# Kernel tuning notes

Measured on AMD Instinct MI355X. Metric: run time of the kernel, lower is better.

## Reference

```python
import jax, jax.numpy as jnp
import numpy as np

NEG = -10000.0
PAD_ID = 0


def setup_inputs() -> dict:
    key = jax.random.key(0)
    ks = jax.random.split(key, 9)
    B, S, D, K, L = 32, 256, 512, 8, 64
    word_rep = jax.random.normal(ks[0], (B, S, D), jnp.float32)
    mask = jnp.ones((B, S), jnp.int32)
    # conv_w[k,:,:,:k+1] are the taps of Conv1d(D, D, k+1); padded to width K for a single tensor
    conv_w = jax.random.normal(ks[1], (K, D, D, K), jnp.float32) * 0.02
    conv_b = jax.random.normal(ks[2], (K, D), jnp.float32) * 0.02
    cls_w = jax.random.normal(ks[3], (L, D), jnp.float32) * 0.02
    cls_b = jax.random.normal(ks[4], (L,), jnp.float32) * 0.02
    T = jax.random.normal(ks[5], (L, L), jnp.float32) * 0.01
    T = T.at[PAD_ID, :].set(NEG).at[:, PAD_ID].set(NEG)
    T_from_BEGIN = jax.random.normal(ks[6], (L,), jnp.float32) * 0.01
    T_from_BEGIN = T_from_BEGIN.at[PAD_ID].set(NEG)
    T_to_END = jax.random.normal(ks[7], (L,), jnp.float32) * 0.01
    T_to_END = T_to_END.at[PAD_ID].set(NEG)
    return dict(word_rep=word_rep, mask=mask, conv_w=conv_w, conv_b=conv_b,
                cls_w=cls_w, cls_b=cls_b, T=T, T_from_BEGIN=T_from_BEGIN, T_to_END=T_to_END)


def _semicrf(word_rep, mask, conv_w, conv_b, cls_w, cls_b, T, T_from_BEGIN, T_to_END):
    B, S, D = word_rep.shape
    K = conv_w.shape[0]
    L = cls_w.shape[0]
    # ---- segment representations: Conv1d(D, D, k+1) placed at [:, k:, k, :] ----
    x = jnp.transpose(word_rep, (0, 2, 1))  # [B, D, S]
    word_seq_rep = jnp.zeros((B, S, K, D), word_rep.dtype)
    for k in range(K):
        w = conv_w[k, :, :, :k + 1]  # [D_out, D_in, k+1]
        out = jax.lax.conv_general_dilated(
            x, w, window_strides=(1,), padding='VALID',
            dimension_numbers=('NCH', 'OIH', 'NCH')) + conv_b[k][None, :, None]  # [B, D, S-k]
        word_seq_rep = word_seq_rep.at[:, k:, k, :].set(jnp.transpose(out, (0, 2, 1)))
    # ---- label scores ----
    label_score = jnp.einsum('bskd,ld->bskl', word_seq_rep, cls_w) + cls_b  # [B,S,K,L]
    label_score = label_score.at[..., PAD_ID].set(NEG)
    seg_ok = jnp.arange(K)[None, :] <= jnp.arange(S)[:, None]  # [S, K]: segment of len k+1 valid only if t >= k
    mask3 = (mask[:, :, None] == 1) & seg_ok[None]              # [B, S, K]
    label_score = jnp.where(mask3[..., None], label_score, NEG)
    # ---- semi-CRF forward recursion over t (sequential scan) ----
    # buf[:, j] holds log_alpha at position t-1-j for j in [0, K)
    def step(buf, inp):
        ls_t, m_t, t = inp  # [B,K,L], [B,K], scalar
        lse_prev = jax.nn.logsumexp(buf, axis=2)                                  # over kk -> [B,K,L']
        tmp = jax.nn.logsumexp(T[None, None, :, :] + lse_prev[:, :, None, :], axis=3)  # over l' -> [B,K,L]
        rec = jnp.where(m_t[..., None], ls_t + tmp, NEG)
        begin = ls_t + T_from_BEGIN[None, None, :]
        karr = jnp.arange(K)[None, :, None]
        row = jnp.where(karr == t, begin, jnp.where(karr > t, NEG, rec))  # [B,K,L]
        buf = jnp.concatenate([row[:, None], buf[:, :-1]], axis=1)
        return buf, row

    buf0 = jnp.full((B, K, K, L), NEG, word_rep.dtype)
    xs = (jnp.transpose(label_score, (1, 0, 2, 3)), jnp.transpose(mask3, (1, 0, 2)), jnp.arange(S))
    _, rows = jax.lax.scan(step, buf0, xs)
    log_alpha = jnp.concatenate(
        [jnp.transpose(rows, (1, 0, 2, 3)), jnp.full((B, 1, K, L), NEG, word_rep.dtype)], axis=1)  # [B,S+1,K,L]
    # ---- log partition: gather log_alpha at last token per segment length, add T_to_END, logsumexp ----
    lengths = jnp.sum(mask, axis=1)                                   # [B]
    idxs = lengths[:, None] - (jnp.arange(K)[None, :] + 1)            # [B,K]
    idxs = jnp.where(idxs >= 0, idxs, S - 1)
    idx_arr = jnp.broadcast_to(idxs[:, None, :, None], (B, 1, K, L))
    g = jnp.take_along_axis(log_alpha, idx_arr, axis=1)[:, 0]         # [B,K,L]
    scores = g + T_to_END[None, None, :]
    return jax.nn.logsumexp(scores.reshape(B, K * L), axis=1)         # [B]


def reference(word_rep, mask, conv_w, conv_b, cls_w, cls_b, T, T_from_BEGIN, T_to_END):
    return _semicrf(word_rep, mask, conv_w, conv_b, cls_w, cls_b, T, T_from_BEGIN, T_to_END)
```

## Files before the change

### kernel.cpp

```cpp
#include <hip/hip_runtime.h>
#include <hip/hip_bf16.h>

#define NEGV (-10000.0f)
constexpr int B_ = 32, S_ = 256, D_ = 512, K_ = 8, L_ = 64;

typedef __bf16 bf16_t;
typedef bf16_t bf16x8 __attribute__((ext_vector_type(8)));
typedef float f32x4 __attribute__((ext_vector_type(4)));

__device__ __forceinline__ float u2f(unsigned int u) {
  union { unsigned int u; float f; } x; x.u = u; return x.f;
}
__device__ __forceinline__ unsigned int f2bfbits(float f) {
  union { bf16_t h; unsigned short u; } x; x.h = (bf16_t)f; return (unsigned int)x.u;
}

__global__ __launch_bounds__(256) void cast_kernel(const float* __restrict__ wr,
                                                   bf16_t* __restrict__ Awr,
                                                   const float* __restrict__ cls_w,
                                                   bf16_t* __restrict__ clsb) {
  const int bid = blockIdx.x;
  if (bid < 2048) {
    const int i = (bid * 256 + threadIdx.x) * 8;
    const float4 a = *(const float4*)(wr + i);
    const float4 b = *(const float4*)(wr + i + 4);
    bf16x8 o;
    o[0] = (bf16_t)a.x; o[1] = (bf16_t)a.y; o[2] = (bf16_t)a.z; o[3] = (bf16_t)a.w;
    o[4] = (bf16_t)b.x; o[5] = (bf16_t)b.y; o[6] = (bf16_t)b.z; o[7] = (bf16_t)b.w;
    *(bf16x8*)(Awr + i) = o;
  } else {
    const int i = ((bid - 2048) * 256 + threadIdx.x) * 8;
    const float4 a = *(const float4*)(cls_w + i);
    const float4 b = *(const float4*)(cls_w + i + 4);
    bf16x8 o;
    o[0] = (bf16_t)a.x; o[1] = (bf16_t)a.y; o[2] = (bf16_t)a.z; o[3] = (bf16_t)a.w;
    o[4] = (bf16_t)b.x; o[5] = (bf16_t)b.y; o[6] = (bf16_t)b.z; o[7] = (bf16_t)b.w;
    *(bf16x8*)(clsb + i) = o;
  }
}

__global__ __launch_bounds__(256) void w2_kernel(const float* __restrict__ conv_w,
                                                 const bf16_t* __restrict__ clsb,
                                                 bf16_t* __restrict__ Vt) {
  const int k = blockIdx.y;
  const int m0 = blockIdx.x * 128;
  const int tid = threadIdx.x;
  const int w = tid >> 6, lane = tid & 63;
  const int wm = w & 1, wn = w >> 1;
  const int lrow = lane & 15, quad = lane >> 4;
  const float* A = conv_w + (size_t)k * 2097152;
  f32x4 acc[4][2] = {};
#pragma unroll 2
  for (int kk = 0; kk < 16; kk++) {
    const int d0 = kk * 32 + quad * 8;
    const bf16x8 b0 = *(const bf16x8*)(clsb + (wn * 32 + lrow) * 512 + kk * 32 + quad * 8);
    const bf16x8 b1 = *(const bf16x8*)(clsb + (wn * 32 + 16 + lrow) * 512 + kk * 32 + quad * 8);
#pragma unroll
    for (int mi = 0; mi < 4; mi++) {
      const int ih = m0 + wm * 64 + mi * 16 + lrow;
      const float* ap = A + (size_t)d0 * 4096 + ih;
      bf16x8 a;
      a[0] = (bf16_t)ap[0 * 4096]; a[1] = (bf16_t)ap[1 * 4096];
      a[2] = (bf16_t)ap[2 * 4096]; a[3] = (bf16_t)ap[3 * 4096];
      a[4] = (bf16_t)ap[4 * 4096]; a[5] = (bf16_t)ap[5 * 4096];
      a[6] = (bf16_t)ap[6 * 4096]; a[7] = (bf16_t)ap[7 * 4096];
      acc[mi][0] = __builtin_amdgcn_mfma_f32_16x16x32_bf16(a, b0, acc[mi][0], 0, 0, 0);
      acc[mi][1] = __builtin_amdgcn_mfma_f32_16x16x32_bf16(a, b1, acc[mi][1], 0, 0, 0);
    }
  }
#pragma unroll
  for (int mi = 0; mi < 4; mi++) {
#pragma unroll
    for (int dd = 0; dd < 4; dd++) {
      const int ih = m0 + wm * 64 + mi * 16 + quad * 4 + dd;
      const int i = ih >> 3, h = ih & 7;
      const int o = k - h;
      if (o >= 0) {
#pragma unroll
        for (int ni = 0; ni < 2; ni++) {
          const int l = wn * 32 + ni * 16 + lrow;
          Vt[(size_t)(k * 64 + l) * 4096 + o * 512 + i] = (bf16_t)acc[mi][ni][dd];
        }
      }
    }
  }
}

__global__ __launch_bounds__(256) void bias2_kernel(const float* __restrict__ conv_b,
                                                    const float* __restrict__ cls_w,
                                                    const float* __restrict__ cls_b,
                                                    float* __restrict__ bias2) {
  const int k = blockIdx.x;
  const int tid = threadIdx.x;
  const int l = tid & 63, c = tid >> 6;
  __shared__ float partb[4][64];
  float s = 0.f;
  for (int d = c * 128; d < c * 128 + 128; d++)
    s += conv_b[k * D_ + d] * cls_w[l * D_ + d];
  partb[c][l] = s;
  __syncthreads();
  if (tid < 64)
    bias2[k * 64 + tid] = cls_b[tid] + partb[0][tid] + partb[1][tid] + partb[2][tid] + partb[3][tid];
}

__global__ __launch_bounds__(256) void ls_mfma(const bf16_t* __restrict__ Awr,
                                               const bf16_t* __restrict__ Vt,
                                               const float* __restrict__ bias2,
                                               const int* __restrict__ mask,
                                               unsigned int* __restrict__ ELSd) {
  constexpr int LDA = 520;
  __shared__ __align__(16) bf16_t As[71 * LDA];
  const int tid = threadIdx.x;
  const int m0 = blockIdx.x * 64;
  const int y = blockIdx.y;
  const int w = tid >> 6, lane = tid & 63;
  const int lrow = lane & 15, quad = lane >> 4;
  const int tblA[4] = {7, 0, 5, 2}, tblB[4] = {6, 1, 4, 3};
  const int kS = (y == 0) ? tblA[w] : tblB[w];

  for (int c = tid; c < 71 * 64; c += 256) {
    const int row = c >> 6, col8 = c & 63;
    int src = m0 - 7 + row;
    if (src < 0) src = 0;
    const uint4 v = *(const uint4*)(Awr + (size_t)src * 512 + col8 * 8);
    *(uint4*)(&As[row * LDA + col8 * 8]) = v;
  }
  __syncthreads();

  f32x4 acc[4][4] = {};
  const int NJ = 16 * (kS + 1);
  const bf16_t* vbase = Vt + (size_t)(kS * 64 + lrow) * 4096 + quad * 8;
#pragma unroll 2
  for (int j = 0; j < NJ; j++) {
    const int o = j >> 4;
    const int col = (j & 15) * 32;
    bf16x8 bfr[4];
#pragma unroll
    for (int ni = 0; ni < 4; ni++)
      bfr[ni] = *(const bf16x8*)(vbase + (size_t)(ni * 16) * 4096 + j * 32);
    const int abase = (lrow + 7 - o) * LDA + col + quad * 8;
#pragma unroll
    for (int mi = 0; mi < 4; mi++) {
      const bf16x8 a = *(const bf16x8*)(&As[abase + mi * 16 * LDA]);
#pragma unroll
      for (int ni = 0; ni < 4; ni++)
        acc[mi][ni] = __builtin_amdgcn_mfma_f32_16x16x32_bf16(a, bfr[ni], acc[mi][ni], 0, 0, 0);
    }
  }

  __syncthreads();
  unsigned short* buf = (unsigned short*)As;
#pragma unroll
  for (int ni = 0; ni < 4; ni++) {
    const int l = ni * 16 + lrow;
    const float bn = bias2[kS * 64 + l];
#pragma unroll
    for (int mi = 0; mi < 4; mi++) {
#pragma unroll
      for (int d = 0; d < 4; d++) {
        const int ml = mi * 16 + quad * 4 + d;
        const int m = m0 + ml;
        const int t = m & 255;
        const bool mok = (mask[m] == 1) && (t >= kS) && (l != 0);
        const float e = mok ? __expf(acc[mi][ni][d] + bn) : 0.f;
        buf[w * 4096 + ml * 64 + l] = (unsigned short)f2bfbits(e);
      }
    }
  }
  __syncthreads();
#pragma unroll
  for (int g = 0; g < 2; g++) {
    const int plane = g * 2 + y;
    const unsigned short* lo = buf + (g * 2) * 4096;
    const unsigned short* hi = buf + (g * 2 + 1) * 4096;
#pragma unroll
    for (int it = 0; it < 16; it++) {
      const int idx = it * 256 + tid;
      const unsigned int dw = (unsigned int)lo[idx] | ((unsigned int)hi[idx] << 16);
      ELSd[((size_t)plane * 8192 + m0 + (idx >> 6)) * 64 + (idx & 63)] = dw;
    }
  }
}

__global__ __launch_bounds__(256, 1) void dp_kernel(const float* __restrict__ T,
                                                    const float* __restrict__ Tfb_g,
                                                    const unsigned int* __restrict__ ELSd,
                                                    float* __restrict__ Mg_lin,
                                                    float* __restrict__ cs_g) {
  const int b = blockIdx.x, tid = threadIdx.x;
  const int w = tid >> 6, l = tid & 63;
  __shared__ __align__(16) float ebuf[64];
  __shared__ float part[4][72];
  __shared__ __align__(16) float pmax[4];
  f32x4 rTq[4];
#pragma unroll
  for (int q = 0; q < 4; q++) {
#pragma unroll
    for (int e = 0; e < 4; e++) rTq[q][e] = __expf(T[l * 64 + w * 16 + q * 4 + e]);
  }
  float mh0 = 0.f, mh1 = 0.f, mh2 = 0.f, mh3 = 0.f, mh4 = 0.f, mh5 = 0.f, mh6 = 0.f, mh7 = 0.f;
  float c = 0.f;
  const unsigned int* e0p = ELSd + ((size_t)0 * 8192 + b * 256) * 64 + l;
  const unsigned int* e1p = ELSd + ((size_t)1 * 8192 + b * 256) * 64 + l;
  const unsigned int* e2p = ELSd + ((size_t)2 * 8192 + b * 256) * 64 + l;
  const unsigned int* e3p = ELSd + ((size_t)3 * 8192 + b * 256) * 64 + l;
  uint4 r0, r1, r2, r3;
  if (w == 0) {
    mh0 = __expf(Tfb_g[l]);
    r0 = make_uint4(e0p[0 * 64], e1p[0 * 64], e2p[0 * 64], e3p[0 * 64]);
    r1 = make_uint4(e0p[1 * 64], e1p[1 * 64], e2p[1 * 64], e3p[1 * 64]);
    r2 = make_uint4(e0p[2 * 64], e1p[2 * 64], e2p[2 * 64], e3p[2 * 64]);
    r3 = make_uint4(e0p[3 * 64], e1p[3 * 64], e2p[3 * 64], e3p[3 * 64]);
  }
  for (int t4 = 0; t4 < 256; t4 += 4) {
#pragma unroll
    for (int u = 0; u < 4; u++) {
      const int t = t4 + u;
      if (w == 0) {
        if (t > 0) {
          const float p0 = part[0][l], p1 = part[1][l], p2 = part[2][l], p3 = part[3][l];
          const float m4 = (p0 + p1) + (p2 + p3);
          if ((t & 3) == 0) {
            const f32x4 pm = *(const f32x4*)pmax;
            float S = fmaxf(fmaxf(pm[0], pm[1]), fmaxf(pm[2], pm[3]));
            S = fmaxf(S, 1e-30f);
            const float inv = __builtin_amdgcn_rcpf(S);
            c += __logf(S);
            mh7 = mh6 * inv; mh6 = mh5 * inv; mh5 = mh4 * inv; mh4 = mh3 * inv;
            mh3 = mh2 * inv; mh2 = mh1 * inv; mh1 = mh0 * inv; mh0 = m4 * inv;
          } else {
            mh7 = mh6; mh6 = mh5; mh5 = mh4; mh4 = mh3;
            mh3 = mh2; mh2 = mh1; mh1 = mh0; mh0 = m4;
          }
        }
        const uint4 q = (u == 0) ? r0 : (u == 1) ? r1 : (u == 2) ? r2 : r3;
        const float f7 = u2f(q.x << 16), fk0 = u2f(q.x & 0xFFFF0000u);
        const float f6 = u2f(q.y << 16), fk1 = u2f(q.y & 0xFFFF0000u);
        const float f5 = u2f(q.z << 16), fk2 = u2f(q.z & 0xFFFF0000u);
        const float f4 = u2f(q.w << 16), fk3 = u2f(q.w & 0xFFFF0000u);
        const float e = ((fk0 * mh0 + fk1 * mh1) + (fk2 * mh2 + fk3 * mh3)) +
                        ((f4 * mh4 + f5 * mh5) + (f6 * mh6 + f7 * mh7));
        ebuf[l] = e;
        int nt = t + 4; if (nt > 255) nt = 255;
        const uint4 nv = make_uint4(e0p[(size_t)nt * 64], e1p[(size_t)nt * 64],
                                    e2p[(size_t)nt * 64], e3p[(size_t)nt * 64]);
        if (u == 0) r0 = nv; else if (u == 1) r1 = nv; else if (u == 2) r2 = nv; else r3 = nv;
      } else if (w == 1) {
        if (t > 0) {
          const float p0 = part[0][l], p1 = part[1][l], p2 = part[2][l], p3 = part[3][l];
          const float m4 = (p0 + p1) + (p2 + p3);
          Mg_lin[((size_t)b * 256 + (t - 1)) * 64 + l] = m4;
          if (l == 0) cs_g[b * 256 + (t - 1)] = c;
          if ((t & 3) == 0) {
            const f32x4 pm = *(const f32x4*)pmax;
            float S = fmaxf(fmaxf(pm[0], pm[1]), fmaxf(pm[2], pm[3]));
            S = fmaxf(S, 1e-30f);
            c += __logf(S);
          }
        }
      }
      __syncthreads();
      {
        const f32x4* evp = (const f32x4*)ebuf;
        const f32x4 v0 = evp[w * 4 + 0], v1 = evp[w * 4 + 1];
        const f32x4 v2 = evp[w * 4 + 2], v3 = evp[w * 4 + 3];
        f32x4 s01 = rTq[0] * v0 + rTq[1] * v1;
        f32x4 s23 = rTq[2] * v2 + rTq[3] * v3;
        const f32x4 sv = s01 + s23;
        part[w][l] = (sv[0] + sv[1]) + (sv[2] + sv[3]);
        const f32x4 mx = __builtin_elementwise_max(__builtin_elementwise_max(v0, v1),
                                                   __builtin_elementwise_max(v2, v3));
        if (l == 0) pmax[w] = fmaxf(fmaxf(mx[0], mx[1]), fmaxf(mx[2], mx[3]));
      }
      __syncthreads();
    }
  }
  if (w == 1) {
    const float p0 = part[0][l], p1 = part[1][l], p2 = part[2][l], p3 = part[3][l];
    const float m4 = (p0 + p1) + (p2 + p3);
    Mg_lin[((size_t)b * 256 + 255) * 64 + l] = m4;
    if (l == 0) cs_g[b * 256 + 255] = c;
  }
}

__global__ __launch_bounds__(64) void final_kernel(const int* __restrict__ mask,
                                                   const float* __restrict__ Tfb_g,
                                                   const float* __restrict__ T2e_g,
                                                   const unsigned int* __restrict__ ELSd,
                                                   const float* __restrict__ Mg_lin,
                                                   const float* __restrict__ cs_g,
                                                   float* __restrict__ out) {
  const int b = blockIdx.x, lane = threadIdx.x;
  int lenp = 0;
  for (int s = lane; s < S_; s += 64) lenp += (mask[b * S_ + s] == 1) ? 1 : 0;
#pragma unroll
  for (int off = 32; off > 0; off >>= 1) lenp += __shfl_xor(lenp, off);
  const int len = lenp;
  const float t2e = T2e_g[lane];
  float vals[8];
  float mx = -3.4e38f;
#pragma unroll
  for (int k = 0; k < 8; k++) {
    int tk = len - 1 - k;
    if (tk < 0) tk = S_ - 1;
    float g;
    if (k > tk) {
      g = NEGV;
    } else {
      const int p = (k < 4) ? k : (7 - k);
      const unsigned int dw = ELSd[((size_t)p * 8192 + b * 256 + tk) * 64 + lane];
      const float elsv = (k < 4) ? u2f(dw & 0xFFFF0000u) : u2f(dw << 16);
      const float ls = (elsv > 0.f) ? __logf(elsv) : NEGV;
      if (k == tk) {
        g = ls + Tfb_g[lane];
      } else if (mask[b * S_ + tk] == 1) {
        const int u = tk - 1 - k;
        const float mlin = Mg_lin[((size_t)b * S_ + u) * 64 + lane];
        const float M = (mlin > 0.f) ? (__logf(mlin) + cs_g[b * S_ + u]) : -1e30f;
        g = ls + M;
      } else {
        g = NEGV;
      }
    }
    const float v = g + t2e;
    vals[k] = v;
    mx = fmaxf(mx, v);
  }
#pragma unroll
  for (int off = 32; off > 0; off >>= 1) mx = fmaxf(mx, __shfl_xor(mx, off));
  float s = 0.f;
#pragma unroll
  for (int k = 0; k < 8; k++) s += __expf(vals[k] - mx);
#pragma unroll
  for (int off = 32; off > 0; off >>= 1) s += __shfl_xor(s, off);
  if (lane == 0) out[b] = __logf(s) + mx;
}

extern "C" void kernel_launch(void* const* d_in, const int* in_sizes, int n_in,
                              void* d_out, int out_size, void* d_ws, size_t ws_size,
                              hipStream_t stream) {
  const float* wr     = (const float*)d_in[0];
  const int*   mask   = (const int*)d_in[1];
  const float* conv_w = (const float*)d_in[2];
  const float* conv_b = (const float*)d_in[3];
  const float* cls_w  = (const float*)d_in[4];
  const float* cls_b  = (const float*)d_in[5];
  const float* T      = (const float*)d_in[6];
  const float* Tfb    = (const float*)d_in[7];
  const float* T2e    = (const float*)d_in[8];
  float* out = (float*)d_out;

  float* ws = (float*)d_ws;
  bf16_t* Vt    = (bf16_t*)ws;
  bf16_t* Awr   = (bf16_t*)(ws + 1048576);
  float*  bias2 = ws + 3145728;
  unsigned int* ELSd = (unsigned int*)(ws + 3146240);
  float*  Mg    = ws + 5243392;
  float*  cs    = ws + 5767680;
  bf16_t* clsb  = (bf16_t*)(ws + 5775872);

  cast_kernel<<<2064, 256, 0, stream>>>(wr, Awr, cls_w, clsb);
  w2_kernel<<<dim3(32, 8), 256, 0, stream>>>(conv_w, clsb, Vt);
  bias2_kernel<<<8, 256, 0, stream>>>(conv_b, cls_w, cls_b, bias2);
  ls_mfma<<<dim3(128, 2), 256, 0, stream>>>(Awr, Vt, bias2, mask, ELSd);
  dp_kernel<<<32, 256, 0, stream>>>(T, Tfb, ELSd, Mg, cs);
  final_kernel<<<32, 64, 0, stream>>>(mask, Tfb, T2e, ELSd, Mg, cs, out);
}
```

Baseline: 304.4 us.

## Fold fp32-to-bf16 casts into consumers and halve ls_mfma row tile

```diff
diff --git a/kernel.cpp b/kernel.cpp
--- a/kernel.cpp
+++ b/kernel.cpp
@@ -14,33 +14,15 @@
 __device__ __forceinline__ unsigned int f2bfbits(float f) {
   union { bf16_t h; unsigned short u; } x; x.h = (bf16_t)f; return (unsigned int)x.u;
 }
-
-__global__ __launch_bounds__(256) void cast_kernel(const float* __restrict__ wr,
-                                                   bf16_t* __restrict__ Awr,
-                                                   const float* __restrict__ cls_w,
-                                                   bf16_t* __restrict__ clsb) {
-  const int bid = blockIdx.x;
-  if (bid < 2048) {
-    const int i = (bid * 256 + threadIdx.x) * 8;
-    const float4 a = *(const float4*)(wr + i);
-    const float4 b = *(const float4*)(wr + i + 4);
-    bf16x8 o;
-    o[0] = (bf16_t)a.x; o[1] = (bf16_t)a.y; o[2] = (bf16_t)a.z; o[3] = (bf16_t)a.w;
-    o[4] = (bf16_t)b.x; o[5] = (bf16_t)b.y; o[6] = (bf16_t)b.z; o[7] = (bf16_t)b.w;
-    *(bf16x8*)(Awr + i) = o;
-  } else {
-    const int i = ((bid - 2048) * 256 + threadIdx.x) * 8;
-    const float4 a = *(const float4*)(cls_w + i);
-    const float4 b = *(const float4*)(cls_w + i + 4);
-    bf16x8 o;
-    o[0] = (bf16_t)a.x; o[1] = (bf16_t)a.y; o[2] = (bf16_t)a.z; o[3] = (bf16_t)a.w;
-    o[4] = (bf16_t)b.x; o[5] = (bf16_t)b.y; o[6] = (bf16_t)b.z; o[7] = (bf16_t)b.w;
-    *(bf16x8*)(clsb + i) = o;
-  }
+__device__ __forceinline__ bf16x8 cvt8(const float4 a, const float4 b) {
+  bf16x8 o;
+  o[0] = (bf16_t)a.x; o[1] = (bf16_t)a.y; o[2] = (bf16_t)a.z; o[3] = (bf16_t)a.w;
+  o[4] = (bf16_t)b.x; o[5] = (bf16_t)b.y; o[6] = (bf16_t)b.z; o[7] = (bf16_t)b.w;
+  return o;
 }
 
 __global__ __launch_bounds__(256) void w2_kernel(const float* __restrict__ conv_w,
-                                                 const bf16_t* __restrict__ clsb,
+                                                 const float* __restrict__ cls_w,
                                                  bf16_t* __restrict__ Vt) {
   const int k = blockIdx.y;
   const int m0 = blockIdx.x * 128;
@@ -53,8 +35,10 @@
 #pragma unroll 2
   for (int kk = 0; kk < 16; kk++) {
     const int d0 = kk * 32 + quad * 8;
-    const bf16x8 b0 = *(const bf16x8*)(clsb + (wn * 32 + lrow) * 512 + kk * 32 + quad * 8);
-    const bf16x8 b1 = *(const bf16x8*)(clsb + (wn * 32 + 16 + lrow) * 512 + kk * 32 + quad * 8);
+    const float* c0p = cls_w + (wn * 32 + lrow) * 512 + kk * 32 + quad * 8;
+    const float* c1p = cls_w + (wn * 32 + 16 + lrow) * 512 + kk * 32 + quad * 8;
+    const bf16x8 b0 = cvt8(*(const float4*)c0p, *(const float4*)(c0p + 4));
+    const bf16x8 b1 = cvt8(*(const float4*)c1p, *(const float4*)(c1p + 4));
 #pragma unroll
     for (int mi = 0; mi < 4; mi++) {
       const int ih = m0 + wm * 64 + mi * 16 + lrow;
@@ -103,31 +87,32 @@
     bias2[k * 64 + tid] = cls_b[tid] + partb[0][tid] + partb[1][tid] + partb[2][tid] + partb[3][tid];
 }
 
-__global__ __launch_bounds__(256) void ls_mfma(const bf16_t* __restrict__ Awr,
+__global__ __launch_bounds__(256) void ls_mfma(const float* __restrict__ wr,
                                                const bf16_t* __restrict__ Vt,
                                                const float* __restrict__ bias2,
                                                const int* __restrict__ mask,
                                                unsigned int* __restrict__ ELSd) {
   constexpr int LDA = 520;
-  __shared__ __align__(16) bf16_t As[71 * LDA];
+  __shared__ __align__(16) bf16_t As[39 * LDA];
   const int tid = threadIdx.x;
-  const int m0 = blockIdx.x * 64;
+  const int m0 = blockIdx.x * 32;
   const int y = blockIdx.y;
   const int w = tid >> 6, lane = tid & 63;
   const int lrow = lane & 15, quad = lane >> 4;
   const int tblA[4] = {7, 0, 5, 2}, tblB[4] = {6, 1, 4, 3};
   const int kS = (y == 0) ? tblA[w] : tblB[w];
 
-  for (int c = tid; c < 71 * 64; c += 256) {
+  for (int c = tid; c < 39 * 64; c += 256) {
     const int row = c >> 6, col8 = c & 63;
     int src = m0 - 7 + row;
     if (src < 0) src = 0;
-    const uint4 v = *(const uint4*)(Awr + (size_t)src * 512 + col8 * 8);
-    *(uint4*)(&As[row * LDA + col8 * 8]) = v;
+    const float* p = wr + (size_t)src * 512 + col8 * 8;
+    const bf16x8 o = cvt8(*(const float4*)p, *(const float4*)(p + 4));
+    *(bf16x8*)(&As[row * LDA + col8 * 8]) = o;
   }
   __syncthreads();
 
-  f32x4 acc[4][4] = {};
+  f32x4 acc[2][4] = {};
   const int NJ = 16 * (kS + 1);
   const bf16_t* vbase = Vt + (size_t)(kS * 64 + lrow) * 4096 + quad * 8;
 #pragma unroll 2
@@ -140,7 +125,7 @@
       bfr[ni] = *(const bf16x8*)(vbase + (size_t)(ni * 16) * 4096 + j * 32);
     const int abase = (lrow + 7 - o) * LDA + col + quad * 8;
 #pragma unroll
-    for (int mi = 0; mi < 4; mi++) {
+    for (int mi = 0; mi < 2; mi++) {
       const bf16x8 a = *(const bf16x8*)(&As[abase + mi * 16 * LDA]);
 #pragma unroll
       for (int ni = 0; ni < 4; ni++)
@@ -155,7 +140,7 @@
     const int l = ni * 16 + lrow;
     const float bn = bias2[kS * 64 + l];
 #pragma unroll
-    for (int mi = 0; mi < 4; mi++) {
+    for (int mi = 0; mi < 2; mi++) {
 #pragma unroll
       for (int d = 0; d < 4; d++) {
         const int ml = mi * 16 + quad * 4 + d;
@@ -163,7 +148,7 @@
         const int t = m & 255;
         const bool mok = (mask[m] == 1) && (t >= kS) && (l != 0);
         const float e = mok ? __expf(acc[mi][ni][d] + bn) : 0.f;
-        buf[w * 4096 + ml * 64 + l] = (unsigned short)f2bfbits(e);
+        buf[w * 2048 + ml * 64 + l] = (unsigned short)f2bfbits(e);
       }
     }
   }
@@ -171,10 +156,10 @@
 #pragma unroll
   for (int g = 0; g < 2; g++) {
     const int plane = g * 2 + y;
-    const unsigned short* lo = buf + (g * 2) * 4096;
-    const unsigned short* hi = buf + (g * 2 + 1) * 4096;
-#pragma unroll
-    for (int it = 0; it < 16; it++) {
+    const unsigned short* lo = buf + (g * 2) * 2048;
+    const unsigned short* hi = buf + (g * 2 + 1) * 2048;
+#pragma unroll
+    for (int it = 0; it < 8; it++) {
       const int idx = it * 256 + tid;
       const unsigned int dw = (unsigned int)lo[idx] | ((unsigned int)hi[idx] << 16);
       ELSd[((size_t)plane * 8192 + m0 + (idx >> 6)) * 64 + (idx & 63)] = dw;
@@ -352,17 +337,14 @@
 
   float* ws = (float*)d_ws;
   bf16_t* Vt    = (bf16_t*)ws;
-  bf16_t* Awr   = (bf16_t*)(ws + 1048576);
-  float*  bias2 = ws + 3145728;
-  unsigned int* ELSd = (unsigned int*)(ws + 3146240);
-  float*  Mg    = ws + 5243392;
-  float*  cs    = ws + 5767680;
-  bf16_t* clsb  = (bf16_t*)(ws + 5775872);
-
-  cast_kernel<<<2064, 256, 0, stream>>>(wr, Awr, cls_w, clsb);
-  w2_kernel<<<dim3(32, 8), 256, 0, stream>>>(conv_w, clsb, Vt);
+  float*  bias2 = ws + 1048576;
+  unsigned int* ELSd = (unsigned int*)(ws + 1049088);
+  float*  Mg    = ws + 3146240;
+  float*  cs    = ws + 3670528;
+
   bias2_kernel<<<8, 256, 0, stream>>>(conv_b, cls_w, cls_b, bias2);
-  ls_mfma<<<dim3(128, 2), 256, 0, stream>>>(Awr, Vt, bias2, mask, ELSd);
+  w2_kernel<<<dim3(32, 8), 256, 0, stream>>>(conv_w, cls_w, Vt);
+  ls_mfma<<<dim3(256, 2), 256, 0, stream>>>(wr, Vt, bias2, mask, ELSd);
   dp_kernel<<<32, 256, 0, stream>>>(T, Tfb, ELSd, Mg, cs);
   final_kernel<<<32, 64, 0, stream>>>(mask, Tfb, T2e, ELSd, Mg, cs, out);
 }
```

After: 311.2 us. 2.2% more time.
